# Kernel tuning notes

Measured on AMD Instinct MI355X. Metric: run time of the kernel, lower is better.

Reference implementation:

```python
import jax, jax.numpy as jnp
import numpy as np

B, T, H, E = 4, 8192, 512, 2048  # batch, seq, hidden (num_dims), embed (num_embeds)
LN_EPS = 1e-5


def _layernorm(x, g, b):
    m = x.mean(-1, keepdims=True)
    v = ((x - m) ** 2).mean(-1, keepdims=True)
    return (x - m) * jax.lax.rsqrt(v + LN_EPS) * g + b


def setup_inputs() -> dict:
    key = jax.random.key(0)
    ks = jax.random.split(key, 8)
    C = 64
    tri = jnp.tril(jnp.ones((C, C), jnp.float32))
    kw = 1.0 / np.sqrt(C)
    inp = {
        "x": jax.random.normal(ks[0], (B, T, H), jnp.float32),
        "ln1_g": jnp.ones((H,), jnp.float32),
        "ln1_b": jnp.zeros((H,), jnp.float32),
        # TriLinear weights: (features, features), lower-triangular masked at init
        "W1": jax.random.uniform(ks[1], (C, C), jnp.float32, -kw, kw) * tri,
        "W2": jax.random.uniform(ks[2], (C, C), jnp.float32, -kw, kw) * tri,
        "ln2_g": jnp.ones((H,), jnp.float32),
        "ln2_b": jnp.zeros((H,), jnp.float32),
        # ffw: Linear(H->E), sin, Linear(E->H); stored (in, out)
        "fw1": jax.random.uniform(ks[3], (H, E), jnp.float32, -1.0 / np.sqrt(H), 1.0 / np.sqrt(H)),
        "fb1": jax.random.uniform(ks[4], (E,), jnp.float32, -1.0 / np.sqrt(H), 1.0 / np.sqrt(H)),
        "fw2": jax.random.uniform(ks[5], (E, H), jnp.float32, -1.0 / np.sqrt(E), 1.0 / np.sqrt(E)),
        "fb2": jax.random.uniform(ks[6], (H,), jnp.float32, -1.0 / np.sqrt(E), 1.0 / np.sqrt(E)),
        "chunk_size": 64,
        "stride": 32,
    }
    return inp


def reference(x, ln1_g, ln1_b, W1, W2, ln2_g, ln2_b, fw1, fb1, fw2, fb2, chunk_size, stride):
    Bb, Tt, Hh = x.shape
    C = chunk_size
    starts = jnp.arange(0, Tt, stride)              # (N,)
    pos = starts[:, None] + jnp.arange(C)           # (N, C)
    valid = (pos < Tt)
    vmask = valid[None, :, :, None].astype(x.dtype)
    safe = jnp.minimum(pos, Tt - 1)
    chunks = x[:, safe] * vmask                     # (B, N, C, H): padded chunks (zeros past T)
    resid = chunks
    cn = _layernorm(chunks, ln1_g, ln1_b)
    tri = jnp.tril(jnp.ones((C, C), x.dtype))
    # TriLinear on time axis (torch transposes to (B,H,C); einsum avoids the transpose)
    y = jnp.einsum('ts,bnsh->bnth', W1 * tri, cn)
    y = jnp.einsum('ts,bnsh->bnth', W2 * tri, y)
    c2 = y + resid
    h = _layernorm(c2, ln2_g, ln2_b)
    h = jnp.sin(h @ fw1 + fb1) @ fw2 + fb2
    out_chunks = (h + c2) * vmask                   # zero the padded tail (torch truncates it)
    flat = safe.reshape(-1)                         # (N*C,)
    out = jnp.zeros_like(x).at[:, flat].add(out_chunks.reshape(Bb, -1, Hh))
    counts = jnp.zeros((Tt,), x.dtype).at[flat].add(valid.reshape(-1).astype(x.dtype))
    return out / jnp.maximum(counts, 1.0)[None, :, None]
```

## Files before the change

kernel.cpp:

```cpp
#include <hip/hip_runtime.h>
#include <math.h>

#define TB 4
#define TT 8192
#define TH 512
#define TE 2048
#define NCHUNK 256
#define GCTOT 1024

typedef unsigned short u16;
typedef short bf8v __attribute__((ext_vector_type(8)));
typedef float f4v __attribute__((ext_vector_type(4)));

__device__ __forceinline__ float bu2f(u16 u) {
    unsigned int x = ((unsigned int)u) << 16; float f; __builtin_memcpy(&f, &x, 4); return f;
}
__device__ __forceinline__ u16 f2bu(float f) {
    unsigned int x; __builtin_memcpy(&x, &f, 4);
    x = x + 0x7fffu + ((x >> 16) & 1u);
    return (u16)(x >> 16);
}

__global__ __launch_bounds__(256) void make_Mt(const float* __restrict__ W1,
                                               const float* __restrict__ W2,
                                               float* __restrict__ Mt) {
    __shared__ float w1[64 * 64];
    __shared__ float w2[64 * 64];
    for (int i = threadIdx.x; i < 4096; i += 256) { w1[i] = W1[i]; w2[i] = W2[i]; }
    __syncthreads();
    for (int i = threadIdx.x; i < 4096; i += 256) {
        int t = i >> 6, s = i & 63;
        float a = 0.f;
        if (t >= s) for (int k = s; k <= t; ++k) a += w2[t * 64 + k] * w1[k * 64 + s];
        Mt[s * 64 + t] = a;
    }
}

__global__ __launch_bounds__(256) void transpose_b(const float* __restrict__ in,
                                                   u16* __restrict__ out, int R, int C) {
    __shared__ u16 tile[64][65];
    const int bx = blockIdx.x, by = blockIdx.y;
    const int tx = threadIdx.x & 63, ty = threadIdx.x >> 6;
#pragma unroll
    for (int i = 0; i < 16; ++i) {
        int r = ty + i * 4;
        tile[r][tx] = f2bu(in[(size_t)(by * 64 + r) * C + bx * 64 + tx]);
    }
    __syncthreads();
#pragma unroll
    for (int i = 0; i < 16; ++i) {
        int r = ty + i * 4;
        out[(size_t)(bx * 64 + r) * R + by * 64 + tx] = tile[tx][r];
    }
}

__global__ __launch_bounds__(256) void ln_stats(const float* __restrict__ x,
                                                float2* __restrict__ st) {
    const int wave = threadIdx.x >> 6, lane = threadIdx.x & 63;
    const size_t row = (size_t)blockIdx.x * 4 + wave;
    const float4* p = (const float4*)(x + row * TH);
    float4 a = p[lane * 2], b = p[lane * 2 + 1];
    float s = 0.f, q = 0.f;
    float v[8] = {a.x, a.y, a.z, a.w, b.x, b.y, b.z, b.w};
#pragma unroll
    for (int i = 0; i < 8; ++i) { s += v[i]; q += v[i] * v[i]; }
#pragma unroll
    for (int o = 32; o; o >>= 1) { s += __shfl_xor(s, o); q += __shfl_xor(q, o); }
    const float mean = s * (1.f / TH);
    float var = q * (1.f / TH) - mean * mean;
    if (var < 0.f) var = 0.f;
    if (lane == 0) st[row] = make_float2(mean, rsqrtf(var + 1e-5f));
}

__global__ __launch_bounds__(256) void ln_rows(const u16* __restrict__ in,
                                               u16* __restrict__ out,
                                               const float* __restrict__ g,
                                               const float* __restrict__ b) {
    const int wave = threadIdx.x >> 6, lane = threadIdx.x & 63;
    const size_t row = (size_t)blockIdx.x * 4 + wave;
    uint4 raw = *((const uint4*)(in + row * TH) + lane);
    const u16* e = (const u16*)&raw;
    float v[8]; float s = 0.f, q = 0.f;
#pragma unroll
    for (int i = 0; i < 8; ++i) { v[i] = bu2f(e[i]); s += v[i]; q += v[i] * v[i]; }
#pragma unroll
    for (int o = 32; o; o >>= 1) { s += __shfl_xor(s, o); q += __shfl_xor(q, o); }
    const float mean = s * (1.f / TH);
    float var = q * (1.f / TH) - mean * mean;
    if (var < 0.f) var = 0.f;
    const float rstd = rsqrtf(var + 1e-5f);
    float4 g0 = ((const float4*)g)[lane * 2], g1 = ((const float4*)g)[lane * 2 + 1];
    float4 b0 = ((const float4*)b)[lane * 2], b1 = ((const float4*)b)[lane * 2 + 1];
    float ge[8] = {g0.x, g0.y, g0.z, g0.w, g1.x, g1.y, g1.z, g1.w};
    float be[8] = {b0.x, b0.y, b0.z, b0.w, b1.x, b1.y, b1.z, b1.w};
    u16 ov[8];
#pragma unroll
    for (int i = 0; i < 8; ++i) ov[i] = f2bu((v[i] - mean) * rstd * ge[i] + be[i]);
    *((uint4*)(out + row * TH) + lane) = *(uint4*)ov;
}

__global__ __launch_bounds__(256) void trilinear_f(const float* __restrict__ x,
                                                   const float2* __restrict__ st,
                                                   const float* __restrict__ g,
                                                   const float* __restrict__ bb,
                                                   const float* __restrict__ Mt,
                                                   u16* __restrict__ c2s,
                                                   int gc0) {
    const int ln = blockIdx.x;
    const int gc = gc0 + ln;
    const int b = gc >> 8, n = gc & 255;
    const int h = (blockIdx.y << 8) + threadIdx.x;
    const int base = n * 32;
    const float gh = g[h], bh = bb[h];
    float acc[64];
#pragma unroll
    for (int t = 0; t < 64; ++t) acc[t] = 0.f;
    for (int s = 0; s < 64; ++s) {
        int pos = base + s; if (pos > TT - 1) pos = TT - 1;
        const size_t ro = (size_t)b * TT + pos;
        const float2 mr = st[ro];
        const float cn = (x[ro * TH + h] - mr.x) * mr.y * gh + bh;
        const float* m = Mt + s * 64;
#pragma unroll
        for (int t = 0; t < 64; ++t) acc[t] += m[t] * cn;
    }
#pragma unroll
    for (int t = 0; t < 64; ++t) {
        int pos = base + t; if (pos > TT - 1) pos = TT - 1;
        const float resid = x[((size_t)b * TT + pos) * TH + h];
        c2s[(size_t)(ln * 64 + t) * TH + h] = f2bu(acc[t] + resid);
    }
}

template <int MODE>
__global__ __launch_bounds__(256) void gemm_bt(const u16* __restrict__ A,
                                               const u16* __restrict__ Bt,
                                               u16* __restrict__ C,
                                               const float* __restrict__ bias,
                                               const u16* __restrict__ addp,
                                               int N, int K) {
    __shared__ u16 lA[128 * 64];
    __shared__ u16 lB[128 * 64];
    const int tid = threadIdx.x;
    const int wave = tid >> 6;
    const int lane = tid & 63;
    const int wr = wave >> 1;
    const int wc = wave & 1;
    const int bm = blockIdx.y << 7;
    const int bn = blockIdx.x << 7;
    const int lrow = lane >> 3;
    const int lcol = (lane & 7) << 3;
    const int fr = lane & 15;
    const int fq = (lane >> 4) << 3;
    f4v acc[4][4] = {};

    for (int kb = 0; kb < K; kb += 64) {
#pragma unroll
        for (int i = 0; i < 4; ++i) {
            const int r = (wave << 5) + (i << 3);
            const u16* ga = A + (size_t)(bm + r + lrow) * K + kb + lcol;
            __builtin_amdgcn_global_load_lds((const __attribute__((address_space(1))) void*)ga,
                                             (__attribute__((address_space(3))) void*)(lA + r * 64),
                                             16, 0, 0);
            const u16* gb = Bt + (size_t)(bn + r + lrow) * K + kb + lcol;
            __builtin_amdgcn_global_load_lds((const __attribute__((address_space(1))) void*)gb,
                                             (__attribute__((address_space(3))) void*)(lB + r * 64),
                                             16, 0, 0);
        }
        __syncthreads();
#pragma unroll
        for (int ks = 0; ks < 64; ks += 32) {
            bf8v af[4], bf[4];
#pragma unroll
            for (int mi = 0; mi < 4; ++mi)
                af[mi] = *(const bf8v*)(lA + ((wr << 6) + (mi << 4) + fr) * 64 + ks + fq);
#pragma unroll
            for (int ni = 0; ni < 4; ++ni)
                bf[ni] = *(const bf8v*)(lB + ((wc << 6) + (ni << 4) + fr) * 64 + ks + fq);
#pragma unroll
            for (int mi = 0; mi < 4; ++mi)
#pragma unroll
                for (int ni = 0; ni < 4; ++ni)
                    acc[mi][ni] = __builtin_amdgcn_mfma_f32_16x16x32_bf16(af[mi], bf[ni], acc[mi][ni], 0, 0, 0);
        }
        __syncthreads();
    }

    const int rq = (lane >> 4) << 2;
#pragma unroll
    for (int mi = 0; mi < 4; ++mi) {
#pragma unroll
        for (int ni = 0; ni < 4; ++ni) {
            const int col = bn + (wc << 6) + (ni << 4) + fr;
            const float bv = bias[col];
#pragma unroll
            for (int r = 0; r < 4; ++r) {
                const int row = bm + (wr << 6) + (mi << 4) + rq + r;
                float v = acc[mi][ni][r] + bv;
                if (MODE == 1) v = __sinf(v);
                else v += bu2f(addp[(size_t)row * N + col]);
                C[(size_t)row * N + col] = f2bu(v);
            }
        }
    }
}

__global__ __launch_bounds__(256) void gather_slice(const u16* __restrict__ ocs,
                                                    const u16* __restrict__ carry,
                                                    float* __restrict__ out,
                                                    int gc0) {
    const int idx = blockIdx.x * 256 + threadIdx.x;
    const int h8 = idx & 63;
    const int prow = idx >> 6;
    const int ap = gc0 * 32 + prow;
    const int b = ap >> 13, t = ap & 8191;
    const int n = t >> 5, c = t & 31;
    const int ln = (b << 8) + n - gc0;
    uint4 r1 = *((const uint4*)ocs + (size_t)(ln * 64 + c) * 64 + h8);
    const u16* e1 = (const u16*)&r1;
    float ov[8];
    if (t < 32) {
#pragma unroll
        for (int i = 0; i < 8; ++i) ov[i] = bu2f(e1[i]);
    } else {
        uint4 r0;
        if (ln == 0) r0 = *((const uint4*)carry + (size_t)(c + 32) * 64 + h8);
        else         r0 = *((const uint4*)ocs + (size_t)((ln - 1) * 64 + c + 32) * 64 + h8);
        const u16* e0 = (const u16*)&r0;
#pragma unroll
        for (int i = 0; i < 8; ++i) ov[i] = 0.5f * (bu2f(e1[i]) + bu2f(e0[i]));
    }
    float4* dst = (float4*)(out + (size_t)ap * TH + h8 * 8);
    dst[0] = make_float4(ov[0], ov[1], ov[2], ov[3]);
    dst[1] = make_float4(ov[4], ov[5], ov[6], ov[7]);
}

__global__ __launch_bounds__(256) void save_carry(const u16* __restrict__ ocs,
                                                  u16* __restrict__ carry, int SC) {
    const int i = blockIdx.x * 256 + threadIdx.x;
    ((uint4*)carry)[i] = ((const uint4*)(ocs + (size_t)(SC - 1) * 64 * TH))[i];
}

extern "C" void kernel_launch(void* const* d_in, const int* in_sizes, int n_in,
                              void* d_out, int out_size, void* d_ws, size_t ws_size,
                              hipStream_t stream) {
    const float* x   = (const float*)d_in[0];
    const float* g1  = (const float*)d_in[1];
    const float* b1  = (const float*)d_in[2];
    const float* W1  = (const float*)d_in[3];
    const float* W2  = (const float*)d_in[4];
    const float* g2  = (const float*)d_in[5];
    const float* b2  = (const float*)d_in[6];
    const float* fw1 = (const float*)d_in[7];
    const float* fb1 = (const float*)d_in[8];
    const float* fw2 = (const float*)d_in[9];
    const float* fb2 = (const float*)d_in[10];
    float* out = (float*)d_out;
    char* ws = (char*)d_ws;

    size_t o = 0;
    auto take = [&](size_t n) { size_t r = o; o = (o + n + 255) & ~(size_t)255; return r; };
    float*  Mt    = (float*) (ws + take(64 * 64 * 4));
    u16*    f1t   = (u16*)   (ws + take((size_t)TE * TH * 2));
    u16*    f2t   = (u16*)   (ws + take((size_t)TH * TE * 2));
    float2* st1   = (float2*)(ws + take((size_t)TB * TT * 8));
    u16*    carry = (u16*)   (ws + take((size_t)64 * TH * 2));
    const size_t fixed = o;

    int SC = 2;
    for (int cand = 256; cand >= 2; cand >>= 1) {
        size_t per = (size_t)cand * 64 * (TH * 2 * 3 + TE * 2) + 4 * 256;
        if (fixed + per <= ws_size) { SC = cand; break; }
    }
    u16* c2s = (u16*)(ws + take((size_t)SC * 64 * TH * 2));
    u16* h2s = (u16*)(ws + take((size_t)SC * 64 * TH * 2));
    u16* ocs = (u16*)(ws + take((size_t)SC * 64 * TH * 2));
    u16* us  = (u16*)(ws + take((size_t)SC * 64 * TE * 2));
    const int SR = SC * 64;

    make_Mt<<<1, 256, 0, stream>>>(W1, W2, Mt);
    transpose_b<<<dim3(TE / 64, TH / 64), 256, 0, stream>>>(fw1, f1t, TH, TE);
    transpose_b<<<dim3(TH / 64, TE / 64), 256, 0, stream>>>(fw2, f2t, TE, TH);
    ln_stats<<<(TB * TT) / 4, 256, 0, stream>>>(x, st1);

    for (int gc0 = 0; gc0 < GCTOT; gc0 += SC) {
        trilinear_f<<<dim3(SC, TH / 256), 256, 0, stream>>>(x, st1, g1, b1, Mt, c2s, gc0);
        ln_rows<<<SR / 4, 256, 0, stream>>>(c2s, h2s, g2, b2);
        gemm_bt<1><<<dim3(TE / 128, SR / 128), 256, 0, stream>>>(
            h2s, f1t, us, fb1, (const u16*)nullptr, TE, TH);
        gemm_bt<2><<<dim3(TH / 128, SR / 128), 256, 0, stream>>>(
            us, f2t, ocs, fb2, c2s, TH, TE);
        gather_slice<<<SC * 8, 256, 0, stream>>>(ocs, carry, out, gc0);
        save_carry<<<16, 256, 0, stream>>>(ocs, carry, SC);
    }
}
```

Before: 806.5 us.

## Double-buffer GEMM LDS tiles with XOR swizzle and block-order remapping

```diff
diff --git a/kernel.cpp b/kernel.cpp
--- a/kernel.cpp
+++ b/kernel.cpp
@@ -133,50 +133,79 @@
 }
 
 template <int MODE>
-__global__ __launch_bounds__(256) void gemm_bt(const u16* __restrict__ A,
+__global__ __launch_bounds__(256) void gemm_db(const u16* __restrict__ A,
                                                const u16* __restrict__ Bt,
                                                u16* __restrict__ C,
                                                const float* __restrict__ bias,
                                                const u16* __restrict__ addp,
                                                int N, int K) {
-    __shared__ u16 lA[128 * 64];
-    __shared__ u16 lB[128 * 64];
+    __shared__ __attribute__((aligned(16))) u16 lA[2][128 * 64];
+    __shared__ __attribute__((aligned(16))) u16 lB[2][128 * 64];
     const int tid = threadIdx.x;
     const int wave = tid >> 6;
     const int lane = tid & 63;
     const int wr = wave >> 1;
     const int wc = wave & 1;
-    const int bm = blockIdx.y << 7;
-    const int bn = blockIdx.x << 7;
-    const int lrow = lane >> 3;
-    const int lcol = (lane & 7) << 3;
     const int fr = lane & 15;
     const int fq = (lane >> 4) << 3;
+    const int s8 = (fr & 7) << 3;
+
+    int bx = blockIdx.x, by = blockIdx.y;
+    const int gx = gridDim.x;
+    const int nwg = gx * (int)gridDim.y;
+    if ((nwg & 7) == 0) {
+        const int bid = by * gx + bx;
+        const int swz = (bid & 7) * (nwg >> 3) + (bid >> 3);
+        bx = swz % gx; by = swz / gx;
+    }
+    const int bm = by << 7;
+    const int bn = bx << 7;
+
+    const int srow = tid >> 3;
+    const int gch = ((tid & 7) ^ (srow & 7)) << 3;
+    const u16* pa = A + (size_t)(bm + srow) * K + gch;
+    const u16* pb = Bt + (size_t)(bn + srow) * K + gch;
+    const int ldsw = wave << 9;
+
+    const int NT = K >> 6;
     f4v acc[4][4] = {};
 
-    for (int kb = 0; kb < K; kb += 64) {
+    auto stage = [&](int t, int buf) {
+        const int ko = t << 6;
 #pragma unroll
         for (int i = 0; i < 4; ++i) {
-            const int r = (wave << 5) + (i << 3);
-            const u16* ga = A + (size_t)(bm + r + lrow) * K + kb + lcol;
-            __builtin_amdgcn_global_load_lds((const __attribute__((address_space(1))) void*)ga,
-                                             (__attribute__((address_space(3))) void*)(lA + r * 64),
-                                             16, 0, 0);
-            const u16* gb = Bt + (size_t)(bn + r + lrow) * K + kb + lcol;
-            __builtin_amdgcn_global_load_lds((const __attribute__((address_space(1))) void*)gb,
-                                             (__attribute__((address_space(3))) void*)(lB + r * 64),
-                                             16, 0, 0);
+            __builtin_amdgcn_global_load_lds(
+                (const __attribute__((address_space(1))) void*)(pa + (size_t)(i * 32) * K + ko),
+                (__attribute__((address_space(3))) void*)(&lA[buf][(i << 11) + ldsw]), 16, 0, 0);
+            __builtin_amdgcn_global_load_lds(
+                (const __attribute__((address_space(1))) void*)(pb + (size_t)(i * 32) * K + ko),
+                (__attribute__((address_space(3))) void*)(&lB[buf][(i << 11) + ldsw]), 16, 0, 0);
         }
-        __syncthreads();
-#pragma unroll
-        for (int ks = 0; ks < 64; ks += 32) {
+    };
+
+    stage(0, 0);
+    __syncthreads();
+
+    const int arow0 = (wr << 6) + fr;
+    const int brow0 = (wc << 6) + fr;
+    const int c0 = fq ^ s8;
+    const int c1 = (32 + fq) ^ s8;
+
+    int buf = 0;
+    for (int t = 0; t < NT; ++t) {
+        if (t + 1 < NT) stage(t + 1, buf ^ 1);
+        const u16* la = lA[buf];
+        const u16* lb = lB[buf];
+#pragma unroll
+        for (int half = 0; half < 2; ++half) {
+            const int cc = half ? c1 : c0;
             bf8v af[4], bf[4];
 #pragma unroll
             for (int mi = 0; mi < 4; ++mi)
-                af[mi] = *(const bf8v*)(lA + ((wr << 6) + (mi << 4) + fr) * 64 + ks + fq);
+                af[mi] = *(const bf8v*)(la + ((arow0 + (mi << 4)) << 6) + cc);
 #pragma unroll
             for (int ni = 0; ni < 4; ++ni)
-                bf[ni] = *(const bf8v*)(lB + ((wc << 6) + (ni << 4) + fr) * 64 + ks + fq);
+                bf[ni] = *(const bf8v*)(lb + ((brow0 + (ni << 4)) << 6) + cc);
 #pragma unroll
             for (int mi = 0; mi < 4; ++mi)
 #pragma unroll
@@ -184,6 +213,7 @@
                     acc[mi][ni] = __builtin_amdgcn_mfma_f32_16x16x32_bf16(af[mi], bf[ni], acc[mi][ni], 0, 0, 0);
         }
         __syncthreads();
+        buf ^= 1;
     }
 
     const int rq = (lane >> 4) << 2;
@@ -286,9 +316,9 @@
     for (int gc0 = 0; gc0 < GCTOT; gc0 += SC) {
         trilinear_f<<<dim3(SC, TH / 256), 256, 0, stream>>>(x, st1, g1, b1, Mt, c2s, gc0);
         ln_rows<<<SR / 4, 256, 0, stream>>>(c2s, h2s, g2, b2);
-        gemm_bt<1><<<dim3(TE / 128, SR / 128), 256, 0, stream>>>(
+        gemm_db<1><<<dim3(TE / 128, SR / 128), 256, 0, stream>>>(
             h2s, f1t, us, fb1, (const u16*)nullptr, TE, TH);
-        gemm_bt<2><<<dim3(TH / 128, SR / 128), 256, 0, stream>>>(
+        gemm_db<2><<<dim3(TH / 128, SR / 128), 256, 0, stream>>>(
             us, f2t, ocs, fb2, c2s, TH, TE);
         gather_slice<<<SC * 8, 256, 0, stream>>>(ocs, carry, out, gc0);
         save_carry<<<16, 256, 0, stream>>>(ocs, carry, SC);
```

Measured after the change: 715.0 us. -11.4%, faster.
